# Kernel optimization log

Measured on AMD Instinct MI355X. Metric: run time of the kernel, lower is better.

## Reference

```python
import jax, jax.numpy as jnp
import numpy as np

EMBED_DIM = 12  # hardcoded in the original module


def setup_inputs() -> dict:
    key = jax.random.key(0)
    k_x, k_w, k_b, k_v = jax.random.split(key, 4)
    feature_dim = 768
    hidden_dim = 4
    feature_num = feature_dim // EMBED_DIM  # 64 fields
    batch = 32768
    x = jax.random.normal(k_x, (batch, feature_dim), dtype=jnp.float32)
    # nn.Linear(feature_dim, 1): weight [1, feature_dim], bias [1]
    W = jax.random.normal(k_w, (1, feature_dim), dtype=jnp.float32) / np.sqrt(feature_dim)
    b = jax.random.normal(k_b, (1,), dtype=jnp.float32) * 0.01
    # V: [feature_num, field_num, hidden_dim]
    V = jax.random.normal(k_v, (feature_num, feature_num, hidden_dim), dtype=jnp.float32)
    return {"x": x, "W": W, "b": b, "V": V}


def reference(x, W, b, V):
    B, D = x.shape
    F = V.shape[0]               # feature_num == field_num
    E = D // F                   # embedding_dim (12)
    # linear part: [B, 1]
    linear_part = x @ W.T + b
    # Pairwise interaction coefficients: C[i, j] = <V[i, j], V[j, i]>
    C = jnp.sum(V * jnp.swapaxes(V, 0, 1), axis=-1)          # [F, F]
    M = C * jnp.triu(jnp.ones((F, F), dtype=x.dtype), k=1)   # keep i < j only
    # sum_{i<j} (x_i . x_j) * C[i,j]  ==  sum_{j,e} Xr[b,j,e] * (sum_i Xr[b,i,e] * M[i,j])
    Xr = x.reshape(B, F, E)                                    # [B, F, E]
    T = jnp.einsum('bie,ij->bje', Xr, M)                       # [B, F, E]
    interaction = jnp.sum(Xr * T, axis=(1, 2))[:, None]        # [B, 1]
    return jax.nn.sigmoid(linear_part + interaction)
```

## Files before the change

### kernel.cpp

```cpp
#include <hip/hip_runtime.h>

#define BATCH   32768
#define DFEAT   768
#define NF      64
#define NE      12
#define NTHR    256
#define RPW     5
#define ROWS_PB (4*RPW)
#define NBLK    ((BATCH + ROWS_PB - 1) / ROWS_PB)
#define PF      8

__global__ void s_prep_kernel(const float* __restrict__ V, float* __restrict__ S) {
    const int idx = blockIdx.x * 256 + threadIdx.x;
    if (idx >= NF * NF) return;
    const int i = idx >> 6, j = idx & 63;
    const float4 a = *(const float4*)(V + (size_t)((i << 6) | j) * 4);
    const float4 b = *(const float4*)(V + (size_t)((j << 6) | i) * 4);
    S[idx] = (i == j) ? 0.0f
           : 0.5f * (a.x * b.x + a.y * b.y + a.z * b.z + a.w * b.w);
}

__global__ __launch_bounds__(NTHR, 4) void ffm_kernel(
    const float* __restrict__ x,
    const float* __restrict__ W,
    const float* __restrict__ bvec,
    const float* __restrict__ S,
    float* __restrict__ out)
{
    __shared__ float red[NTHR];

    const int tid  = threadIdx.x;
    const int w    = tid >> 6;
    const int lane = tid & 63;
    const int r    = lane / NE;
    const int e    = lane - r * NE;

    int row = blockIdx.x * ROWS_PB + w * RPW + (r < RPW ? r : 0);
    if (row >= BATCH) row = BATCH - 1;

    const float* xrow = x + (size_t)row * DFEAT + e;

    float acc[NF];
    #pragma unroll
    for (int j = 0; j < NF; ++j) acc[j] = 0.0f;

    float xbuf[PF];
    #pragma unroll
    for (int u = 0; u < PF; ++u) xbuf[u] = xrow[u * NE];

    for (int i8 = 0; i8 < NF; i8 += PF) {
        #pragma unroll
        for (int u = 0; u < PF; ++u) {
            const int i = i8 + u;
            const float xv = xbuf[u];
            const float* srow = S + i * NF;
            #pragma unroll
            for (int j = 0; j < NF; ++j)
                acc[j] = fmaf(srow[j], xv, acc[j]);
            const int inext = (i + PF < NF) ? (i + PF) : (NF - 1);
            xbuf[u] = xrow[inext * NE];
        }
    }

    float p = 0.0f;
    #pragma unroll
    for (int j = 0; j < NF; ++j) {
        const float xj = xrow[j * NE];
        const float wj = W[j * NE + e];
        p = fmaf(xj, acc[j] + wj, p);
    }

    red[tid] = p;
    __syncthreads();

    if (tid < ROWS_PB) {
        const int w2 = tid / RPW, r2 = tid - w2 * RPW;
        const int orow = blockIdx.x * ROWS_PB + w2 * RPW + r2;
        if (orow < BATCH) {
            float s = 0.0f;
            #pragma unroll
            for (int q = 0; q < NE; ++q) s += red[(w2 << 6) + r2 * NE + q];
            const float z = s + bvec[0];
            out[orow] = 1.0f / (1.0f + __expf(-z));
        }
    }
}

extern "C" void kernel_launch(void* const* d_in, const int* in_sizes, int n_in,
                              void* d_out, int out_size, void* d_ws, size_t ws_size,
                              hipStream_t stream) {
    const float* x  = (const float*)d_in[0];
    const float* W  = (const float*)d_in[1];
    const float* bb = (const float*)d_in[2];
    const float* V  = (const float*)d_in[3];
    float* S   = (float*)d_ws;
    float* out = (float*)d_out;

    s_prep_kernel<<<dim3((NF * NF + 255) / 256), dim3(256), 0, stream>>>(V, S);
    ffm_kernel<<<dim3(NBLK), dim3(NTHR), 0, stream>>>(x, W, bb, S, out);
}
```

Baseline: 172.4 us.

## Compute field interaction with split-bf16 MFMA matrix cores instead of scalar FMAs

```diff
diff --git a/kernel.cpp b/kernel.cpp
--- a/kernel.cpp
+++ b/kernel.cpp
@@ -1,88 +1,166 @@
 #include <hip/hip_runtime.h>
+#include <hip/hip_bf16.h>
 
-#define BATCH   32768
-#define DFEAT   768
-#define NF      64
-#define NE      12
-#define NTHR    256
-#define RPW     5
-#define ROWS_PB (4*RPW)
-#define NBLK    ((BATCH + ROWS_PB - 1) / ROWS_PB)
-#define PF      8
+#define BATCH 32768
+#define NF    64
+#define NE    12
+#define MB    16
+#define MROWS (MB*NE)
+#define LSTR  68
+#define NBLK  (BATCH/MB)
 
-__global__ void s_prep_kernel(const float* __restrict__ V, float* __restrict__ S) {
-    const int idx = blockIdx.x * 256 + threadIdx.x;
-    if (idx >= NF * NF) return;
-    const int i = idx >> 6, j = idx & 63;
-    const float4 a = *(const float4*)(V + (size_t)((i << 6) | j) * 4);
-    const float4 b = *(const float4*)(V + (size_t)((j << 6) | i) * 4);
-    S[idx] = (i == j) ? 0.0f
-           : 0.5f * (a.x * b.x + a.y * b.y + a.z * b.z + a.w * b.w);
+typedef __attribute__((ext_vector_type(8))) short short8;
+typedef __attribute__((ext_vector_type(4))) float float4v;
+
+#define WS_SHT 0
+#define WS_SLT 8192
+#define WS_WT  16384
+
+__device__ __forceinline__ short bfb(float v) {
+    union { __hip_bfloat16 h; short s; } u;
+    u.h = __float2bfloat16(v);
+    return u.s;
 }
 
-__global__ __launch_bounds__(NTHR, 4) void ffm_kernel(
+__global__ void prep_kernel(const float* __restrict__ V, const float* __restrict__ W,
+                            unsigned short* __restrict__ ShT,
+                            unsigned short* __restrict__ SlT,
+                            float* __restrict__ WT) {
+    const int idx = blockIdx.x * 256 + threadIdx.x;
+    if (idx < NF * NF) {
+        const int i = idx >> 6, j = idx & 63;
+        const float4v a = *(const float4v*)(V + (size_t)((i << 6) | j) * 4);
+        const float4v b = *(const float4v*)(V + (size_t)((j << 6) | i) * 4);
+        const float s = (i == j) ? 0.0f
+                      : 0.5f * (a.x * b.x + a.y * b.y + a.z * b.z + a.w * b.w);
+        const __hip_bfloat16 sh = __float2bfloat16(s);
+        const float shf = __bfloat162float(sh);
+        union { __hip_bfloat16 h; unsigned short u; } uh, ul;
+        uh.h = sh; ul.h = __float2bfloat16(s - shf);
+        ShT[(j << 6) | i] = uh.u;
+        SlT[(j << 6) | i] = ul.u;
+    }
+    if (idx < NF * NE) {
+        const int j = idx / NE, e = idx - j * NE;
+        WT[e * 64 + j] = W[idx];
+    }
+}
+
+__global__ __launch_bounds__(256, 3) void ffm_mfma(
     const float* __restrict__ x,
-    const float* __restrict__ W,
     const float* __restrict__ bvec,
-    const float* __restrict__ S,
+    const unsigned short* __restrict__ ShT,
+    const unsigned short* __restrict__ SlT,
+    const float* __restrict__ WT,
     float* __restrict__ out)
 {
-    __shared__ float red[NTHR];
+    __shared__ float Xs[MROWS * LSTR];
+    __shared__ float red[MROWS];
 
     const int tid  = threadIdx.x;
     const int w    = tid >> 6;
     const int lane = tid & 63;
-    const int r    = lane / NE;
-    const int e    = lane - r * NE;
+    const int l15  = lane & 15;
+    const int q    = lane >> 4;
 
-    int row = blockIdx.x * ROWS_PB + w * RPW + (r < RPW ? r : 0);
-    if (row >= BATCH) row = BATCH - 1;
+    short8 shf[4][2], slf[4][2];
+    #pragma unroll
+    for (int ns = 0; ns < 4; ++ns)
+        #pragma unroll
+        for (int kb = 0; kb < 2; ++kb) {
+            const int off = ((ns << 4) + l15) * 64 + kb * 32 + q * 8;
+            shf[ns][kb] = *(const short8*)(ShT + off);
+            slf[ns][kb] = *(const short8*)(SlT + off);
+        }
 
-    const float* xrow = x + (size_t)row * DFEAT + e;
+    const float4v* xg = (const float4v*)(x + (size_t)blockIdx.x * MB * (NF * NE));
+    #pragma unroll
+    for (int p = 0; p < 12; ++p) {
+        const int fid = p * 256 + tid;
+        const int b   = fid / 192;
+        const int c4  = fid - b * 192;
+        const float4v v = xg[fid];
+        const int d0 = c4 * 4;
+        const int i0 = d0 / 12;
+        const int e0 = d0 - i0 * 12;
+        float* dst = Xs + (b * NE + e0) * LSTR + i0;
+        dst[0 * LSTR] = v.x; dst[1 * LSTR] = v.y;
+        dst[2 * LSTR] = v.z; dst[3 * LSTR] = v.w;
+    }
+    __syncthreads();
 
-    float acc[NF];
+    float4v acc[3][4];
     #pragma unroll
-    for (int j = 0; j < NF; ++j) acc[j] = 0.0f;
+    for (int ms = 0; ms < 3; ++ms)
+        #pragma unroll
+        for (int ns = 0; ns < 4; ++ns)
+            acc[ms][ns] = (float4v){0.f, 0.f, 0.f, 0.f};
 
-    float xbuf[PF];
     #pragma unroll
-    for (int u = 0; u < PF; ++u) xbuf[u] = xrow[u * NE];
-
-    for (int i8 = 0; i8 < NF; i8 += PF) {
+    for (int ms = 0; ms < 3; ++ms) {
+        const int msg  = w * 3 + ms;
+        const int mrow = (msg << 4) + l15;
+        float av[16];
         #pragma unroll
-        for (int u = 0; u < PF; ++u) {
-            const int i = i8 + u;
-            const float xv = xbuf[u];
-            const float* srow = S + i * NF;
+        for (int kb = 0; kb < 2; ++kb) {
+            const float4v t0 = *(const float4v*)(Xs + mrow * LSTR + kb * 32 + q * 8);
+            const float4v t1 = *(const float4v*)(Xs + mrow * LSTR + kb * 32 + q * 8 + 4);
+            av[kb*8+0]=t0.x; av[kb*8+1]=t0.y; av[kb*8+2]=t0.z; av[kb*8+3]=t0.w;
+            av[kb*8+4]=t1.x; av[kb*8+5]=t1.y; av[kb*8+6]=t1.z; av[kb*8+7]=t1.w;
+        }
+        short8 ah[2], al[2];
+        #pragma unroll
+        for (int kb = 0; kb < 2; ++kb)
             #pragma unroll
-            for (int j = 0; j < NF; ++j)
-                acc[j] = fmaf(srow[j], xv, acc[j]);
-            const int inext = (i + PF < NF) ? (i + PF) : (NF - 1);
-            xbuf[u] = xrow[inext * NE];
+            for (int j = 0; j < 8; ++j) {
+                const float v = av[kb * 8 + j];
+                const __hip_bfloat16 h = __float2bfloat16(v);
+                const float r = v - __bfloat162float(h);
+                ah[kb][j] = bfb(v) , al[kb][j] = bfb(r);
+            }
+        #pragma unroll
+        for (int ns = 0; ns < 4; ++ns) {
+            float4v c = acc[ms][ns];
+            c = __builtin_amdgcn_mfma_f32_16x16x32_bf16(ah[0], shf[ns][0], c, 0, 0, 0);
+            c = __builtin_amdgcn_mfma_f32_16x16x32_bf16(ah[1], shf[ns][1], c, 0, 0, 0);
+            c = __builtin_amdgcn_mfma_f32_16x16x32_bf16(al[0], shf[ns][0], c, 0, 0, 0);
+            c = __builtin_amdgcn_mfma_f32_16x16x32_bf16(al[1], shf[ns][1], c, 0, 0, 0);
+            c = __builtin_amdgcn_mfma_f32_16x16x32_bf16(ah[0], slf[ns][0], c, 0, 0, 0);
+            c = __builtin_amdgcn_mfma_f32_16x16x32_bf16(ah[1], slf[ns][1], c, 0, 0, 0);
+            acc[ms][ns] = c;
         }
     }
 
-    float p = 0.0f;
     #pragma unroll
-    for (int j = 0; j < NF; ++j) {
-        const float xj = xrow[j * NE];
-        const float wj = W[j * NE + e];
-        p = fmaf(xj, acc[j] + wj, p);
+    for (int ms = 0; ms < 3; ++ms) {
+        const int msg = w * 3 + ms;
+        #pragma unroll
+        for (int rg = 0; rg < 4; ++rg) {
+            const int m = (msg << 4) + (q << 2) + rg;
+            const int e = m % NE;
+            float p = 0.0f;
+            #pragma unroll
+            for (int ns = 0; ns < 4; ++ns) {
+                const int n = (ns << 4) + l15;
+                const float a  = Xs[m * LSTR + n];
+                const float wt = WT[e * 64 + n];
+                p = fmaf(a, acc[ms][ns][rg] + wt, p);
+            }
+            p += __shfl_xor(p, 1);
+            p += __shfl_xor(p, 2);
+            p += __shfl_xor(p, 4);
+            p += __shfl_xor(p, 8);
+            if (l15 == 0) red[m] = p;
+        }
     }
-
-    red[tid] = p;
     __syncthreads();
 
-    if (tid < ROWS_PB) {
-        const int w2 = tid / RPW, r2 = tid - w2 * RPW;
-        const int orow = blockIdx.x * ROWS_PB + w2 * RPW + r2;
-        if (orow < BATCH) {
-            float s = 0.0f;
-            #pragma unroll
-            for (int q = 0; q < NE; ++q) s += red[(w2 << 6) + r2 * NE + q];
-            const float z = s + bvec[0];
-            out[orow] = 1.0f / (1.0f + __expf(-z));
-        }
+    if (tid < MB) {
+        float s = 0.0f;
+        #pragma unroll
+        for (int e = 0; e < NE; ++e) s += red[tid * NE + e];
+        const float z = s + bvec[0];
+        out[blockIdx.x * MB + tid] = 1.0f / (1.0f + __expf(-z));
     }
 }
 
@@ -93,9 +171,11 @@
     const float* W  = (const float*)d_in[1];
     const float* bb = (const float*)d_in[2];
     const float* V  = (const float*)d_in[3];
-    float* S   = (float*)d_ws;
+    unsigned short* ShT = (unsigned short*)((char*)d_ws + WS_SHT);
+    unsigned short* SlT = (unsigned short*)((char*)d_ws + WS_SLT);
+    float*          WT  = (float*)((char*)d_ws + WS_WT);
     float* out = (float*)d_out;
 
-    s_prep_kernel<<<dim3((NF * NF + 255) / 256), dim3(256), 0, stream>>>(V, S);
-    ffm_kernel<<<dim3(NBLK), dim3(NTHR), 0, stream>>>(x, W, bb, S, out);
+    prep_kernel<<<dim3(16), dim3(256), 0, stream>>>(V, W, ShT, SlT, WT);
+    ffm_mfma<<<dim3(NBLK), dim3(256), 0, stream>>>(x, bb, ShT, SlT, WT, out);
 }
```

Result: faster. 163.1 us (-5.4%).
